# Optimization experiments

Measured on AMD Instinct MI355X. Metric: run time of the kernel, lower is better.

The kernel has to match this reference:

```python
import jax, jax.numpy as jnp
import numpy as np

B, N, T_OBS, N_HEAD = 64, 512, 8, 4
IN_FEAT = T_OBS * 2          # 16
OUT_FEAT = IN_FEAT * 4       # 64 (GAT out / MLP in)
HID1, HID2 = 1024, 512
S, NSAMP = 2, 20
OUT_DIM = S * NSAMP          # 40


def setup_inputs() -> dict:
    key = jax.random.key(0)
    ks = jax.random.split(key, 12)
    x = jax.random.normal(ks[0], (B, N, T_OBS, 2), dtype=jnp.float32)
    # binary adjacency-style mask over the dense node-node attention
    mask = (jax.random.uniform(ks[1], (B, 1, N, N)) > 0.1).astype(jnp.float32)
    xav = lambda k, shp, fi, fo: jax.random.uniform(k, shp, jnp.float32, -1.0, 1.0) * (1.414 * np.sqrt(6.0 / (fi + fo)))
    w = xav(ks[2], (N_HEAD, IN_FEAT, OUT_FEAT), IN_FEAT, OUT_FEAT)
    a_src = xav(ks[3], (N_HEAD, OUT_FEAT, 1), OUT_FEAT, 1)
    a_dst = xav(ks[4], (N_HEAD, OUT_FEAT, 1), OUT_FEAT, 1)
    bias = jnp.zeros((OUT_FEAT,), jnp.float32)
    lin = lambda k, fi, fo: jax.random.uniform(k, (fi, fo), jnp.float32, -1.0, 1.0) * np.sqrt(1.0 / fi)
    W1 = lin(ks[5], OUT_FEAT, HID1); b1 = jnp.zeros((HID1,), jnp.float32)
    W2 = lin(ks[6], HID1, HID2);     b2 = jnp.zeros((HID2,), jnp.float32)
    W3 = lin(ks[7], HID2, OUT_DIM);  b3 = jnp.zeros((OUT_DIM,), jnp.float32)
    return {"x": x, "mask": mask, "w": w, "a_src": a_src, "a_dst": a_dst,
            "bias": bias, "W1": W1, "b1": b1, "W2": W2, "b2": b2, "W3": W3, "b3": b3}


def reference(x, mask, w, a_src, a_dst, bias, W1, b1, W2, b2, W3, b3):
    b, n = x.shape[0], x.shape[1]
    node = x.reshape(b, n, -1)                                   # [B,N,16]
    # per-head projection: [B,N,16] x [H,16,64] -> [B,H,N,64]
    h_prime = jnp.einsum('bni,hio->bhno', node, w)
    attn_src = jnp.einsum('bhno,ho->bhn', h_prime, a_src[..., 0])
    attn_dst = jnp.einsum('bhno,ho->bhn', h_prime, a_dst[..., 0])
    attn = attn_src[..., :, None] * attn_dst[..., None, :]       # [B,H,N,N] outer product
    attn = jnp.where(attn >= 0, attn, 0.2 * attn)                # leaky_relu(0.2)
    attn = jax.nn.softmax(attn, axis=-1)
    # dropout is identity in eval mode
    attn = attn * mask
    out = jnp.einsum('bhnm,bhmo->bno', attn, h_prime) + bias     # sum over heads fused
    out = out + h_prime.sum(axis=1)                              # skip connection
    # MLP: activation BEFORE each linear (as in original MLP.forward)
    y = out
    for W, bb in ((W1, b1), (W2, b2), (W3, b3)):
        y = jax.nn.relu(y) @ W + bb
    y = y.reshape(b, n, NSAMP, -1)[..., 0:S]                     # [B,N,20,2]
    return jnp.clip(jax.nn.sigmoid(y), 0.01, 0.99)
```

## Files before the change

kernel.cpp:

```cpp
#include <hip/hip_runtime.h>
#include <math.h>

typedef short bf16x8 __attribute__((ext_vector_type(8)));
typedef float f32x4 __attribute__((ext_vector_type(4)));

#define BB 64
#define NN 512
#define NH 4
#define FI 16
#define FO 64
#define HD1 1024
#define HD2 512
#define ODIM 40

__device__ __forceinline__ unsigned short f2bf(float f) {
    unsigned u = __float_as_uint(f);
    u += 0x7fffu + ((u >> 16) & 1u);
    return (unsigned short)(u >> 16);
}
__device__ __forceinline__ unsigned pack2(float a, float b) {
    return (unsigned)f2bf(a) | ((unsigned)f2bf(b) << 16);
}
__device__ __forceinline__ void gload16(const void* g, void* l) {
    __builtin_amdgcn_global_load_lds(
        (const __attribute__((address_space(1))) unsigned int*)g,
        (__attribute__((address_space(3))) unsigned int*)l,
        16, 0, 0);
}

__global__ void k_wa(const float* __restrict__ w, const float* __restrict__ a_src,
                     const float* __restrict__ a_dst, float* __restrict__ wa)
{
    int t = threadIdx.x;
    int h = t >> 4;
    float s = 0.f, d = 0.f;
    for (int o = 0; o < FO; ++o) {
        float wv = w[t*FO + o];
        s = fmaf(wv, a_src[h*FO + o], s);
        d = fmaf(wv, a_dst[h*FO + o], d);
    }
    wa[t] = s; wa[64 + t] = d;
}

__global__ __launch_bounds__(256) void k_proj2(
    const float* __restrict__ x, const float* __restrict__ w,
    const float* __restrict__ bias, const float* __restrict__ wa,
    short* __restrict__ hpT,
    float* __restrict__ asrc, float* __restrict__ adst,
    float* __restrict__ gat)
{
    __shared__ float xS[64][20];
    __shared__ float gS[NH][64][64];
    int b = blockIdx.y;
    int n0 = blockIdx.x * 64;
    int t = threadIdx.x;
    int h = t >> 6, o = t & 63;
    {
        int n = t >> 2, q = t & 3;
        float4 v = *(const float4*)&x[((size_t)b*NN + n0 + n)*FI + q*4];
        *(float4*)&xS[n][q*4] = v;
    }
    float wreg[16];
#pragma unroll
    for (int i = 0; i < FI; ++i) wreg[i] = w[(h*FI + i)*FO + o];
    __syncthreads();

    short* hb = hpT + (size_t)b * (NH*FO*NN);
    for (int nc = 0; nc < 8; ++nc) {
        float acc[8];
#pragma unroll
        for (int k = 0; k < 8; ++k) {
            int n = nc*8 + k;
            float4 a0 = *(const float4*)&xS[n][0];
            float4 a1 = *(const float4*)&xS[n][4];
            float4 a2 = *(const float4*)&xS[n][8];
            float4 a3 = *(const float4*)&xS[n][12];
            float sA = fmaf(a0.x, wreg[0], fmaf(a0.y, wreg[1], fmaf(a0.z, wreg[2], a0.w*wreg[3])));
            float sB = fmaf(a1.x, wreg[4], fmaf(a1.y, wreg[5], fmaf(a1.z, wreg[6], a1.w*wreg[7])));
            float sC = fmaf(a2.x, wreg[8], fmaf(a2.y, wreg[9], fmaf(a2.z, wreg[10], a2.w*wreg[11])));
            float sD = fmaf(a3.x, wreg[12], fmaf(a3.y, wreg[13], fmaf(a3.z, wreg[14], a3.w*wreg[15])));
            float s = (sA + sB) + (sC + sD);
            acc[k] = s;
            gS[h][n][o] = s;
        }
        uint4 p;
        p.x = pack2(acc[0], acc[1]); p.y = pack2(acc[2], acc[3]);
        p.z = pack2(acc[4], acc[5]); p.w = pack2(acc[6], acc[7]);
        int jt = (n0 >> 5) + (nc >> 2);
        *(uint4*)&hb[(size_t)(jt*256 + h*64 + o)*32 + (nc & 3)*8] = p;
    }
    {
        int n = o;
        float vs = 0.f, vd = 0.f;
#pragma unroll
        for (int i = 0; i < FI; ++i) {
            float xv = xS[n][i];
            vs = fmaf(xv, wa[h*FI + i], vs);
            vd = fmaf(xv, wa[64 + h*FI + i], vd);
        }
        asrc[(size_t)(b*NH + h)*NN + n0 + n] = vs;
        adst[(size_t)(b*NH + h)*NN + n0 + n] = vd;
    }
    __syncthreads();
#pragma unroll
    for (int r = 0; r < 16; ++r) {
        int idx = t + r*256;
        int n = idx >> 6, oo = idx & 63;
        float g = bias[oo] + ((gS[0][n][oo] + gS[1][n][oo]) + (gS[2][n][oo] + gS[3][n][oo]));
        gat[((size_t)b*NN + n0 + n)*FO + oo] = g;
    }
}

__global__ __launch_bounds__(256) void k_attn2(
    const short* __restrict__ hpT, const float* __restrict__ mask,
    const float* __restrict__ asrc, const float* __restrict__ adst,
    float* __restrict__ gat)
{
    __shared__ float dS[NH*NN];
    __shared__ float dmaxS[NH], dminS[NH];
    int b = blockIdx.y;
    int i0blk = blockIdx.x * 64;
    int t = threadIdx.x;
#pragma unroll
    for (int r = 0; r < 8; ++r) {
        int idx = t + r*256;
        dS[idx] = adst[(size_t)b*(NH*NN) + idx];
    }
    __syncthreads();
    int wv = t >> 6, lane = t & 63;
    {
        float mx = -INFINITY, mn = INFINITY;
        const float* dh = &dS[wv*NN];
#pragma unroll
        for (int q = 0; q < 8; ++q) {
            float v = dh[lane*8 + q];
            mx = fmaxf(mx, v); mn = fminf(mn, v);
        }
#pragma unroll
        for (int off = 1; off < 64; off <<= 1) {
            mx = fmaxf(mx, __shfl_xor(mx, off));
            mn = fminf(mn, __shfl_xor(mn, off));
        }
        if (lane == 0) { dmaxS[wv] = mx; dminS[wv] = mn; }
    }
    __syncthreads();
    int li = lane & 15, kq = lane >> 4;
    int i = i0blk + wv*16 + li;
    float s[NH], m[NH], Ssum[NH];
#pragma unroll
    for (int h = 0; h < NH; ++h) {
        s[h] = asrc[(size_t)(b*NH + h)*NN + i];
        float dm = s[h] >= 0.f ? dmaxS[h] : dminS[h];
        float l = s[h] * dm;
        m[h] = fmaxf(l, 0.2f*l);
        Ssum[h] = 0.f;
    }
    f32x4 accH[NH][4];
#pragma unroll
    for (int h = 0; h < NH; ++h)
#pragma unroll
        for (int ot = 0; ot < 4; ++ot) accH[h][ot] = (f32x4)0.f;

    const float* mrow = &mask[((size_t)b*NN + i)*NN];
    const short* vb = hpT + (size_t)b * (NH*FO*NN);
    for (int jt = 0; jt < 16; ++jt) {
        int j0 = jt*32;
        float4 mk0 = *(const float4*)&mrow[j0 + kq*8];
        float4 mk1 = *(const float4*)&mrow[j0 + kq*8 + 4];
        float mk[8] = {mk0.x, mk0.y, mk0.z, mk0.w, mk1.x, mk1.y, mk1.z, mk1.w};
#pragma unroll
        for (int h = 0; h < NH; ++h) {
            float4 d0 = *(const float4*)&dS[h*NN + j0 + kq*8];
            float4 d1 = *(const float4*)&dS[h*NN + j0 + kq*8 + 4];
            float dv[8] = {d0.x,d0.y,d0.z,d0.w,d1.x,d1.y,d1.z,d1.w};
            float u[8];
#pragma unroll
            for (int q = 0; q < 8; ++q) {
                float v = s[h]*dv[q];
                v = fmaxf(v, 0.2f*v);
                u[q] = __expf(v - m[h]);
            }
            Ssum[h] += ((u[0]+u[1]) + (u[2]+u[3])) + ((u[4]+u[5]) + (u[6]+u[7]));
            union { bf16x8 v; unsigned uu[4]; } pf;
#pragma unroll
            for (int q = 0; q < 4; ++q)
                pf.uu[q] = pack2(u[2*q]*mk[2*q], u[2*q+1]*mk[2*q+1]);
#pragma unroll
            for (int ot = 0; ot < 4; ++ot) {
                bf16x8 vf = *(const bf16x8*)&vb[(size_t)(jt*256 + h*64 + ot*16 + li)*32 + kq*8];
                accH[h][ot] = __builtin_amdgcn_mfma_f32_16x16x32_bf16(pf.v, vf, accH[h][ot], 0, 0, 0);
            }
        }
    }
#pragma unroll
    for (int h = 0; h < NH; ++h) {
        Ssum[h] += __shfl_xor(Ssum[h], 16);
        Ssum[h] += __shfl_xor(Ssum[h], 32);
    }
    float rinv[NH][4];
#pragma unroll
    for (int h = 0; h < NH; ++h)
#pragma unroll
        for (int g = 0; g < 4; ++g)
            rinv[h][g] = 1.0f / __shfl(Ssum[h], kq*4 + g);
#pragma unroll
    for (int ot = 0; ot < 4; ++ot) {
#pragma unroll
        for (int g = 0; g < 4; ++g) {
            int ii = i0blk + wv*16 + kq*4 + g;
            int oo = ot*16 + li;
            size_t ix = ((size_t)b*NN + ii)*FO + oo;
            float add = accH[0][ot][g]*rinv[0][g] + accH[1][ot][g]*rinv[1][g]
                      + accH[2][ot][g]*rinv[2][g] + accH[3][ot][g]*rinv[3][g];
            gat[ix] += add;
        }
    }
}

__global__ __launch_bounds__(256) void k_conv(
    const float* __restrict__ W1, const float* __restrict__ W2, const float* __restrict__ W3,
    short* __restrict__ w1t, short* __restrict__ w2f, short* __restrict__ w3t)
{
    int idx = blockIdx.x * 256 + threadIdx.x;
    if (idx < HD1*FO) {
        int n = idx >> 6, k = idx & 63;
        w1t[idx] = (short)f2bf(W1[k*HD1 + n]);
    } else if (idx < HD1*FO + HD2*HD1) {
        int i2 = idx - HD1*FO;
        int e = i2 & 7, kqq = (i2 >> 3) & 3, n = (i2 >> 5) & 511, ks = i2 >> 14;
        int k = ks*32 + kqq*8 + e;
        w2f[i2] = (short)f2bf(W2[k*HD2 + n]);
    } else if (idx < HD1*FO + HD2*HD1 + 48*HD2) {
        int i3 = idx - (HD1*FO + HD2*HD1);
        int n = i3 >> 9, k = i3 & 511;
        w3t[i3] = (short)(n < ODIM ? f2bf(W3[k*ODIM + n]) : 0);
    }
}

__global__ __launch_bounds__(256, 2) void k_mlpA(
    const float* __restrict__ gat,
    const short* __restrict__ w1t, const float* __restrict__ b1,
    short* __restrict__ h1g)
{
    __shared__ char a0b[8192];
    int t = threadIdx.x;
    int lane = t & 63, wave = t >> 6;
    int li = lane & 15, kq = lane >> 4;
    int m0 = blockIdx.x * 64;

    {
        int row = t >> 2, c0 = (t & 3) * 16;
        const float4* g = (const float4*)&gat[(size_t)(m0 + row) * FO + c0];
        float4 v0 = g[0], v1 = g[1], v2 = g[2], v3 = g[3];
        uint4 p0, p1;
        p0.x = pack2(fmaxf(v0.x,0.f), fmaxf(v0.y,0.f));
        p0.y = pack2(fmaxf(v0.z,0.f), fmaxf(v0.w,0.f));
        p0.z = pack2(fmaxf(v1.x,0.f), fmaxf(v1.y,0.f));
        p0.w = pack2(fmaxf(v1.z,0.f), fmaxf(v1.w,0.f));
        p1.x = pack2(fmaxf(v2.x,0.f), fmaxf(v2.y,0.f));
        p1.y = pack2(fmaxf(v2.z,0.f), fmaxf(v2.w,0.f));
        p1.z = pack2(fmaxf(v3.x,0.f), fmaxf(v3.y,0.f));
        p1.w = pack2(fmaxf(v3.z,0.f), fmaxf(v3.w,0.f));
        int base = row*128 + c0*2;
        *(uint4*)(a0b + (base ^ ((row&7)<<4)))      = p0;
        *(uint4*)(a0b + ((base+16) ^ ((row&7)<<4))) = p1;
    }
    __syncthreads();

    for (int c = 0; c < 4; ++c) {
        int n0 = wave * 256 + c * 64;
        f32x4 acc[4][4];
#pragma unroll
        for (int mt = 0; mt < 4; ++mt)
#pragma unroll
            for (int nt = 0; nt < 4; ++nt) acc[mt][nt] = (f32x4)0.f;
#pragma unroll
        for (int ks = 0; ks < 2; ++ks) {
            int k0 = ks * 32;
            bf16x8 xf[4];
#pragma unroll
            for (int mt = 0; mt < 4; ++mt) {
                int row = mt * 16 + li;
                int addr = (row * 128 + k0 * 2 + kq * 16) ^ ((row & 7) << 4);
                xf[mt] = *(bf16x8*)(a0b + addr);
            }
#pragma unroll
            for (int nt = 0; nt < 4; ++nt) {
                int col = n0 + nt * 16 + li;
                bf16x8 wf = *(const bf16x8*)(w1t + col * 64 + k0 + kq * 8);
#pragma unroll
                for (int mt = 0; mt < 4; ++mt)
                    acc[mt][nt] = __builtin_amdgcn_mfma_f32_16x16x32_bf16(wf, xf[mt], acc[mt][nt], 0, 0, 0);
            }
        }
#pragma unroll
        for (int mt = 0; mt < 4; ++mt)
#pragma unroll
            for (int nt = 0; nt < 4; ++nt) {
                int m = mt * 16 + li;
                int nb = n0 + nt * 16 + kq * 4;
                float4 bb = *(const float4*)&b1[nb];
                float v0 = fmaxf(acc[mt][nt][0] + bb.x, 0.f);
                float v1 = fmaxf(acc[mt][nt][1] + bb.y, 0.f);
                float v2 = fmaxf(acc[mt][nt][2] + bb.z, 0.f);
                float v3 = fmaxf(acc[mt][nt][3] + bb.w, 0.f);
                uint2 pw; pw.x = pack2(v0, v1); pw.y = pack2(v2, v3);
                *(uint2*)&h1g[(size_t)(m0 + m) * HD1 + nb] = pw;
            }
    }
}

__global__ __launch_bounds__(512, 2) void k_mlpB(
    const short* __restrict__ h1g,
    const short* __restrict__ w2f, const float* __restrict__ b2,
    const short* __restrict__ w3t, const float* __restrict__ b3,
    float* __restrict__ out)
{
    extern __shared__ char smem[];
    int t = threadIdx.x;
    int lane = t & 63, wave = t >> 6;
    int li = lane & 15, kq = lane >> 4;
    int m0 = blockIdx.x * 128;

    auto STAGE = [&](int i, int ks) {
        char* base = smem + i * 8192;
        int row = wave * 16 + (lane >> 2);
        int slotS = (lane & 3) ^ ((row >> 1) & 3);
        const short* src = h1g + (size_t)(m0 + row) * HD1 + ks * 32 + slotS * 8;
        gload16(src, base + wave * 1024);
    };
    const short* wfbase = w2f + ((size_t)(wave*64 + li)*4 + kq)*8;

    f32x4 acc2[8][4];
#pragma unroll
    for (int mt = 0; mt < 8; ++mt)
#pragma unroll
        for (int nt = 0; nt < 4; ++nt) acc2[mt][nt] = (f32x4)0.f;

    bf16x8 wf0[4], wf1[4];
    __builtin_amdgcn_sched_barrier(0);
    STAGE(0, 0);
#pragma unroll
    for (int nt = 0; nt < 4; ++nt) wf0[nt] = *(const bf16x8*)(wfbase + 0*16384 + nt*512);
    __builtin_amdgcn_sched_barrier(0);
    STAGE(1, 1);
#pragma unroll
    for (int nt = 0; nt < 4; ++nt) wf1[nt] = *(const bf16x8*)(wfbase + 1*16384 + nt*512);
    __builtin_amdgcn_sched_barrier(0);

    for (int ks = 0; ks < 32; ++ks) {
        int cur = ks & 1;
        if (ks < 31) { asm volatile("s_waitcnt vmcnt(5)" ::: "memory"); }
        else         { asm volatile("s_waitcnt vmcnt(0)" ::: "memory"); }
        __builtin_amdgcn_sched_barrier(0);
        __builtin_amdgcn_s_barrier();
        __builtin_amdgcn_sched_barrier(0);

        char* base = smem + cur * 8192;
        bf16x8 xf[8];
#pragma unroll
        for (int mt = 0; mt < 8; ++mt) {
            int m = mt * 16 + li;
            int slot = kq ^ ((m >> 1) & 3);
            xf[mt] = *(bf16x8*)(base + m * 64 + slot * 16);
        }
        asm volatile("s_waitcnt lgkmcnt(0)" ::: "memory");
        __builtin_amdgcn_sched_barrier(0);
        __builtin_amdgcn_s_barrier();
        __builtin_amdgcn_sched_barrier(0);

        bf16x8 wfn[4];
        if (ks < 30) {
            STAGE(cur, ks + 2);
#pragma unroll
            for (int nt = 0; nt < 4; ++nt)
                wfn[nt] = *(const bf16x8*)(wfbase + (size_t)(ks+2)*16384 + nt*512);
        }
        __builtin_amdgcn_sched_barrier(0);

#pragma unroll
        for (int nt = 0; nt < 4; ++nt)
#pragma unroll
            for (int mt = 0; mt < 8; ++mt)
                acc2[mt][nt] = __builtin_amdgcn_mfma_f32_16x16x32_bf16(wf0[nt], xf[mt], acc2[mt][nt], 0, 0, 0);
        if (ks < 30) {
#pragma unroll
            for (int nt = 0; nt < 4; ++nt) { wf0[nt] = wf1[nt]; wf1[nt] = wfn[nt]; }
        } else {
#pragma unroll
            for (int nt = 0; nt < 4; ++nt) wf0[nt] = wf1[nt];
        }
    }
    __syncthreads();

#pragma unroll
    for (int mt = 0; mt < 8; ++mt)
#pragma unroll
        for (int nt = 0; nt < 4; ++nt) {
            int m = mt * 16 + li;
            int nb = wave * 64 + nt * 16 + kq * 4;
            float4 bb = *(const float4*)&b2[nb];
            float v0 = fmaxf(acc2[mt][nt][0] + bb.x, 0.f);
            float v1 = fmaxf(acc2[mt][nt][1] + bb.y, 0.f);
            float v2 = fmaxf(acc2[mt][nt][2] + bb.z, 0.f);
            float v3 = fmaxf(acc2[mt][nt][3] + bb.w, 0.f);
            uint2 pw; pw.x = pack2(v0, v1); pw.y = pack2(v2, v3);
            int addr = (m * 1024 + nb * 2) ^ ((m & 7) << 4);
            *(uint2*)(smem + addr) = pw;
        }
    __syncthreads();

    f32x4 acc3[3];
#pragma unroll
    for (int nt = 0; nt < 3; ++nt) acc3[nt] = (f32x4)0.f;
#pragma unroll
    for (int ks = 0; ks < 16; ++ks) {
        int k0 = ks * 32;
        int m = wave * 16 + li;
        int addr = (m * 1024 + k0 * 2 + kq * 16) ^ ((m & 7) << 4);
        bf16x8 xf = *(bf16x8*)(smem + addr);
#pragma unroll
        for (int nt = 0; nt < 3; ++nt) {
            int col = nt * 16 + li;
            bf16x8 wf = *(const bf16x8*)(w3t + col * 512 + k0 + kq * 8);
            acc3[nt] = __builtin_amdgcn_mfma_f32_16x16x32_bf16(wf, xf, acc3[nt], 0, 0, 0);
        }
    }
#pragma unroll
    for (int nt = 0; nt < 3; ++nt)
#pragma unroll
        for (int g = 0; g < 4; ++g) {
            int n = nt * 16 + kq * 4 + g;
            if (n < ODIM) {
                int m = wave * 16 + li;
                float s = acc3[nt][g] + b3[n];
                s = 1.f / (1.f + __expf(-s));
                s = fminf(fmaxf(s, 0.01f), 0.99f);
                out[(size_t)(m0 + m) * ODIM + n] = s;
            }
        }
}

extern "C" void kernel_launch(void* const* d_in, const int* in_sizes, int n_in,
                              void* d_out, int out_size, void* d_ws, size_t ws_size,
                              hipStream_t stream)
{
    const float* x     = (const float*)d_in[0];
    const float* mask  = (const float*)d_in[1];
    const float* w     = (const float*)d_in[2];
    const float* a_src = (const float*)d_in[3];
    const float* a_dst = (const float*)d_in[4];
    const float* bias  = (const float*)d_in[5];
    const float* W1    = (const float*)d_in[6];
    const float* b1    = (const float*)d_in[7];
    const float* W2    = (const float*)d_in[8];
    const float* b2    = (const float*)d_in[9];
    const float* W3    = (const float*)d_in[10];
    const float* b3    = (const float*)d_in[11];
    float* out = (float*)d_out;

    char* p = (char*)d_ws;
    short* h1g = (short*)p;
    short* hpT = (short*)p;  p += (size_t)BB*NH*FO*NN*2;
    float* asrc = (float*)p; p += (size_t)BB*NH*NN*4;
    float* adst = (float*)p; p += (size_t)BB*NH*NN*4;
    p = (char*)d_ws + (size_t)BB*NN*HD1*2;
    float* gat  = (float*)p; p += (size_t)BB*NN*FO*4;
    short* w1t  = (short*)p; p += (size_t)HD1*FO*2;
    short* w2f  = (short*)p; p += (size_t)HD2*HD1*2;
    short* w3t  = (short*)p; p += (size_t)48*HD2*2;
    float* wa   = (float*)p; p += 128*4;

    k_wa   <<<1, 64, 0, stream>>>(w, a_src, a_dst, wa);
    k_conv <<<(HD1*FO + HD2*HD1 + 48*HD2)/256, 256, 0, stream>>>(W1, W2, W3, w1t, w2f, w3t);
    k_proj2<<<dim3(NN/64, BB), 256, 0, stream>>>(x, w, bias, wa, hpT, asrc, adst, gat);
    k_attn2<<<dim3(NN/64, BB), 256, 0, stream>>>(hpT, mask, asrc, adst, gat);
    k_mlpA <<<BB*NN/64, 256, 0, stream>>>(gat, w1t, b1, h1g);
    k_mlpB <<<BB*NN/128, 512, 131072, stream>>>(h1g, w2f, b2, w3t, b3, out);
}
```

Before: 168.3 us.

## Split attention key range across two wave groups with LDS reduction

The attention kernel now runs 512 threads per block: two groups of four waves each process half of the key range (256 columns) for the same 64 query rows. Partial MFMA accumulators and softmax sums are combined through shared memory before normalisation and the write to gat. The mask loads are also software-prefetched one tile ahead. This doubles wave-level parallelism per block to hide latency, at the cost of about 64KB of extra LDS, an extra barrier and a reduction step, and register pressure under launch_bounds(512,4).

```diff
diff --git a/kernel.cpp b/kernel.cpp
--- a/kernel.cpp
+++ b/kernel.cpp
@@ -111,26 +111,29 @@
     }
 }
 
-__global__ __launch_bounds__(256) void k_attn2(
+__global__ __launch_bounds__(512, 4) void k_attn2(
     const short* __restrict__ hpT, const float* __restrict__ mask,
     const float* __restrict__ asrc, const float* __restrict__ adst,
     float* __restrict__ gat)
 {
     __shared__ float dS[NH*NN];
     __shared__ float dmaxS[NH], dminS[NH];
+    __shared__ float part[NH*NH*4*64*4];
+    __shared__ float ssp[4*NH*64];
     int b = blockIdx.y;
     int i0blk = blockIdx.x * 64;
     int t = threadIdx.x;
 #pragma unroll
-    for (int r = 0; r < 8; ++r) {
-        int idx = t + r*256;
+    for (int r = 0; r < 4; ++r) {
+        int idx = t + r*512;
         dS[idx] = adst[(size_t)b*(NH*NN) + idx];
     }
     __syncthreads();
-    int wv = t >> 6, lane = t & 63;
-    {
+    int wave = t >> 6, lane = t & 63;
+    int wv4 = wave & 3, jh = wave >> 2;
+    if (wave < 4) {
         float mx = -INFINITY, mn = INFINITY;
-        const float* dh = &dS[wv*NN];
+        const float* dh = &dS[wave*NN];
 #pragma unroll
         for (int q = 0; q < 8; ++q) {
             float v = dh[lane*8 + q];
@@ -141,11 +144,11 @@
             mx = fmaxf(mx, __shfl_xor(mx, off));
             mn = fminf(mn, __shfl_xor(mn, off));
         }
-        if (lane == 0) { dmaxS[wv] = mx; dminS[wv] = mn; }
+        if (lane == 0) { dmaxS[wave] = mx; dminS[wave] = mn; }
     }
     __syncthreads();
     int li = lane & 15, kq = lane >> 4;
-    int i = i0blk + wv*16 + li;
+    int i = i0blk + wv4*16 + li;
     float s[NH], m[NH], Ssum[NH];
 #pragma unroll
     for (int h = 0; h < NH; ++h) {
@@ -163,11 +166,17 @@
 
     const float* mrow = &mask[((size_t)b*NN + i)*NN];
     const short* vb = hpT + (size_t)b * (NH*FO*NN);
-    for (int jt = 0; jt < 16; ++jt) {
+    float4 mk0 = *(const float4*)&mrow[jh*256 + kq*8];
+    float4 mk1 = *(const float4*)&mrow[jh*256 + kq*8 + 4];
+    for (int jtt = 0; jtt < 8; ++jtt) {
+        int jt = jh*8 + jtt;
+        float4 c0 = mk0, c1 = mk1;
+        if (jtt < 7) {
+            mk0 = *(const float4*)&mrow[(jt+1)*32 + kq*8];
+            mk1 = *(const float4*)&mrow[(jt+1)*32 + kq*8 + 4];
+        }
         int j0 = jt*32;
-        float4 mk0 = *(const float4*)&mrow[j0 + kq*8];
-        float4 mk1 = *(const float4*)&mrow[j0 + kq*8 + 4];
-        float mk[8] = {mk0.x, mk0.y, mk0.z, mk0.w, mk1.x, mk1.y, mk1.z, mk1.w};
+        float mk[8] = {c0.x, c0.y, c0.z, c0.w, c1.x, c1.y, c1.z, c1.w};
 #pragma unroll
         for (int h = 0; h < NH; ++h) {
             float4 d0 = *(const float4*)&dS[h*NN + j0 + kq*8];
@@ -192,27 +201,51 @@
             }
         }
     }
-#pragma unroll
-    for (int h = 0; h < NH; ++h) {
-        Ssum[h] += __shfl_xor(Ssum[h], 16);
-        Ssum[h] += __shfl_xor(Ssum[h], 32);
-    }
-    float rinv[NH][4];
-#pragma unroll
-    for (int h = 0; h < NH; ++h)
-#pragma unroll
-        for (int g = 0; g < 4; ++g)
-            rinv[h][g] = 1.0f / __shfl(Ssum[h], kq*4 + g);
-#pragma unroll
-    for (int ot = 0; ot < 4; ++ot) {
-#pragma unroll
-        for (int g = 0; g < 4; ++g) {
-            int ii = i0blk + wv*16 + kq*4 + g;
-            int oo = ot*16 + li;
-            size_t ix = ((size_t)b*NN + ii)*FO + oo;
-            float add = accH[0][ot][g]*rinv[0][g] + accH[1][ot][g]*rinv[1][g]
-                      + accH[2][ot][g]*rinv[2][g] + accH[3][ot][g]*rinv[3][g];
-            gat[ix] += add;
+    if (jh == 0) {
+#pragma unroll
+        for (int h = 0; h < NH; ++h) {
+#pragma unroll
+            for (int ot = 0; ot < 4; ++ot) {
+                float4 v = {accH[h][ot][0], accH[h][ot][1], accH[h][ot][2], accH[h][ot][3]};
+                *(float4*)&part[(((wv4*NH + h)*4 + ot)*64 + lane)*4] = v;
+            }
+            ssp[(wv4*NH + h)*64 + lane] = Ssum[h];
+        }
+    }
+    __syncthreads();
+    if (jh == 1) {
+#pragma unroll
+        for (int h = 0; h < NH; ++h) {
+#pragma unroll
+            for (int ot = 0; ot < 4; ++ot) {
+                float4 p = *(const float4*)&part[(((wv4*NH + h)*4 + ot)*64 + lane)*4];
+                accH[h][ot][0] += p.x; accH[h][ot][1] += p.y;
+                accH[h][ot][2] += p.z; accH[h][ot][3] += p.w;
+            }
+            Ssum[h] += ssp[(wv4*NH + h)*64 + lane];
+        }
+#pragma unroll
+        for (int h = 0; h < NH; ++h) {
+            Ssum[h] += __shfl_xor(Ssum[h], 16);
+            Ssum[h] += __shfl_xor(Ssum[h], 32);
+        }
+        float rinv[NH][4];
+#pragma unroll
+        for (int h = 0; h < NH; ++h)
+#pragma unroll
+            for (int g = 0; g < 4; ++g)
+                rinv[h][g] = 1.0f / __shfl(Ssum[h], kq*4 + g);
+#pragma unroll
+        for (int ot = 0; ot < 4; ++ot) {
+#pragma unroll
+            for (int g = 0; g < 4; ++g) {
+                int ii = i0blk + wv4*16 + kq*4 + g;
+                int oo = ot*16 + li;
+                size_t ix = ((size_t)b*NN + ii)*FO + oo;
+                float add = accH[0][ot][g]*rinv[0][g] + accH[1][ot][g]*rinv[1][g]
+                          + accH[2][ot][g]*rinv[2][g] + accH[3][ot][g]*rinv[3][g];
+                gat[ix] += add;
+            }
         }
     }
 }
@@ -474,7 +507,7 @@
     k_wa   <<<1, 64, 0, stream>>>(w, a_src, a_dst, wa);
     k_conv <<<(HD1*FO + HD2*HD1 + 48*HD2)/256, 256, 0, stream>>>(W1, W2, W3, w1t, w2f, w3t);
     k_proj2<<<dim3(NN/64, BB), 256, 0, stream>>>(x, w, bias, wa, hpT, asrc, adst, gat);
-    k_attn2<<<dim3(NN/64, BB), 256, 0, stream>>>(hpT, mask, asrc, adst, gat);
+    k_attn2<<<dim3(NN/64, BB), 512, 0, stream>>>(hpT, mask, asrc, adst, gat);
     k_mlpA <<<BB*NN/64, 256, 0, stream>>>(gat, w1t, b1, h1g);
     k_mlpB <<<BB*NN/128, 512, 131072, stream>>>(h1g, w2f, b2, w3t, b3, out);
 }
```

Result: slower. 210.7 us (+25.2%).
